# Optimization experiments

Measured on AMD Instinct MI355X. Metric: run time of the kernel, lower is better.

The kernel has to match this reference:

```python
import jax, jax.numpy as jnp
import numpy as np

VOCAB, EMB, HID = 32000, 1024, 1024
T, B = 256, 16
SIGMA = 0.01


def setup_inputs() -> dict:
    key = jax.random.key(0)
    ks = jax.random.split(key, 5)
    X = jax.random.randint(ks[0], (T, B), 0, VOCAB)
    W_e = jax.random.normal(ks[1], (VOCAB, EMB), dtype=jnp.float32) * SIGMA
    W_xh = jax.random.normal(ks[2], (EMB, HID), dtype=jnp.float32) * SIGMA
    W_hh = jax.random.normal(ks[3], (HID, HID), dtype=jnp.float32) * SIGMA
    b_h = jnp.zeros((HID,), dtype=jnp.float32)
    W_hq = jax.random.normal(ks[4], (HID, VOCAB), dtype=jnp.float32) * SIGMA
    b_q = jnp.zeros((VOCAB,), dtype=jnp.float32)
    return {"X": X, "W_e": W_e, "W_xh": W_xh, "W_hh": W_hh, "b_h": b_h,
            "W_hq": W_hq, "b_q": b_q}


def reference(X, W_e, W_xh, W_hh, b_h, W_hq, b_q):
    # one_hot(X) @ W_e is mathematically a row gather
    emb = W_e[X]  # [T, B, E]
    h0 = jnp.zeros((X.shape[1], W_hh.shape[0]), dtype=W_e.dtype)

    def step(h, x_t):
        h = jnp.tanh(x_t @ W_xh + h @ W_hh + b_h)
        return h, h

    _, hidden_states = jax.lax.scan(step, h0, emb)  # [T, B, H]
    logits = jnp.einsum('tbh,hv->tbv', hidden_states, W_hq) + b_q  # [T, B, V]
    return logits
```

## Files before the change

kernel.cpp:

```cpp
#include <hip/hip_runtime.h>
#include <hip/hip_bf16.h>
#include <stdint.h>

#define T_STEPS 256
#define BATCH   16
#define HIDDIM  1024
#define VOCAB   32000
#define TB      4096

typedef __attribute__((ext_vector_type(8))) short  short8;
typedef __attribute__((ext_vector_type(4))) float  floatx4;

__device__ inline unsigned short f2bfu(float x) {
  __hip_bfloat16 h = __float2bfloat16(x);
  unsigned short u;
  __builtin_memcpy(&u, &h, 2);
  return u;
}
__device__ inline float bfu2f(unsigned short u) {
  __hip_bfloat16 h;
  __builtin_memcpy(&h, &u, 2);
  return __bfloat162float(h);
}

__global__ __launch_bounds__(256) void transpose_cvt(
    const float* __restrict__ src, unsigned short* __restrict__ dst,
    unsigned short* __restrict__ dst_lo, int K, int N) {
  __shared__ float tile[64][65];
  int n0 = blockIdx.x * 64, k0 = blockIdx.y * 64;
  int tid = threadIdx.x;
#pragma unroll
  for (int j = 0; j < 16; ++j) {
    int idx = j * 256 + tid;
    int kl = idx >> 6, nl = idx & 63;
    tile[kl][nl] = src[(size_t)(k0 + kl) * N + n0 + nl];
  }
  __syncthreads();
#pragma unroll
  for (int j = 0; j < 16; ++j) {
    int idx = j * 256 + tid;
    int nl = idx >> 6, kl = idx & 63;
    float v = tile[kl][nl];
    unsigned short hi = f2bfu(v);
    dst[(size_t)(n0 + nl) * K + k0 + kl] = hi;
    if (dst_lo) dst_lo[(size_t)(n0 + nl) * K + k0 + kl] = f2bfu(v - bfu2f(hi));
  }
}

__global__ __launch_bounds__(256) void gather_cvt(
    const int* __restrict__ X, const float* __restrict__ We,
    unsigned short* __restrict__ emb) {
  int r = blockIdx.x;
  int row = X[r];
  int c = threadIdx.x * 4;
  float4 v = *(const float4*)(We + (size_t)row * HIDDIM + c);
  ushort4 o;
  o.x = f2bfu(v.x); o.y = f2bfu(v.y); o.z = f2bfu(v.z); o.w = f2bfu(v.w);
  *(ushort4*)(emb + (size_t)r * HIDDIM + c) = o;
}

#define BM 128
#define BN 128
#define BK 64

__device__ inline void glds16(const unsigned short* gp, unsigned short* lp) {
  __builtin_amdgcn_global_load_lds(
      (__attribute__((address_space(1))) unsigned int*)(uintptr_t)gp,
      (__attribute__((address_space(3))) unsigned int*)(unsigned int)(uintptr_t)lp,
      16, 0, 0);
}

__global__ __launch_bounds__(256) void gemm_bf16(
    const unsigned short* __restrict__ A,
    const unsigned short* __restrict__ BT,
    const float* __restrict__ bias,
    float* __restrict__ C,
    int N, int K) {
  __shared__ unsigned short As[BM * BK];
  __shared__ unsigned short Bs[BN * BK];
  int tid = threadIdx.x;
  int wave = tid >> 6, lane = tid & 63;
  int l15 = lane & 15, quad = lane >> 4;
  int m0 = blockIdx.y * BM, n0 = blockIdx.x * BN;
  int wm = (wave >> 1) * 64, wn = (wave & 1) * 64;
  int lrow = lane >> 3, lk = (lane & 7) * 8;
  floatx4 acc[4][4] = {};
  for (int kt = 0; kt < K; kt += BK) {
    __syncthreads();
#pragma unroll
    for (int i = 0; i < 4; ++i) {
      int rb = wave * 32 + i * 8;
      glds16(A  + (size_t)(m0 + rb + lrow) * K + kt + lk, As + rb * BK);
      glds16(BT + (size_t)(n0 + rb + lrow) * K + kt + lk, Bs + rb * BK);
    }
    __syncthreads();
#pragma unroll
    for (int ks = 0; ks < 2; ++ks) {
      short8 af[4], bv[4];
#pragma unroll
      for (int i = 0; i < 4; ++i)
        af[i] = *(const short8*)(As + (wm + i * 16 + l15) * BK + ks * 32 + quad * 8);
#pragma unroll
      for (int i = 0; i < 4; ++i)
        bv[i] = *(const short8*)(Bs + (wn + i * 16 + l15) * BK + ks * 32 + quad * 8);
#pragma unroll
      for (int mt = 0; mt < 4; ++mt)
#pragma unroll
        for (int nt = 0; nt < 4; ++nt)
          acc[mt][nt] = __builtin_amdgcn_mfma_f32_16x16x32_bf16(af[mt], bv[nt], acc[mt][nt], 0, 0, 0);
    }
  }
#pragma unroll
  for (int nt = 0; nt < 4; ++nt) {
    int gn = n0 + wn + nt * 16 + l15;
    float bvv = bias ? bias[gn] : 0.0f;
#pragma unroll
    for (int mt = 0; mt < 4; ++mt) {
      int gm = m0 + wm + mt * 16 + quad * 4;
#pragma unroll
      for (int r = 0; r < 4; ++r)
        C[(size_t)(gm + r) * N + gn] = acc[mt][nt][r] + bvv;
    }
  }
}

#define SCAN_WGS 64

__device__ inline short8 ld_h16_agent(const unsigned long long* p) {
  unsigned long long a = __hip_atomic_load(p,     __ATOMIC_RELAXED, __HIP_MEMORY_SCOPE_AGENT);
  unsigned long long b = __hip_atomic_load(p + 1, __ATOMIC_RELAXED, __HIP_MEMORY_SCOPE_AGENT);
  union { unsigned long long u[2]; short8 s; } c;
  c.u[0] = a; c.u[1] = b;
  return c.s;
}

__global__ __launch_bounds__(64) void scan_kernel(
    const float* __restrict__ pre,
    const unsigned short* __restrict__ WThi,
    const unsigned short* __restrict__ WTlo,
    unsigned short* __restrict__ h_hi,
    unsigned short* __restrict__ h_lo,
    unsigned int* __restrict__ flags) {
  int lane = threadIdx.x;
  int l15 = lane & 15, quad = lane >> 4;
  int wg = blockIdx.x;
  int mslice = wg * 16;
  short8 Ahi[32], Alo[32];
  {
    const unsigned short* wh = WThi + (size_t)(mslice + l15) * HIDDIM + quad * 8;
    const unsigned short* wl = WTlo + (size_t)(mslice + l15) * HIDDIM + quad * 8;
#pragma unroll
    for (int kt = 0; kt < 32; ++kt) {
      Ahi[kt] = *(const short8*)(wh + kt * 32);
      Alo[kt] = *(const short8*)(wl + kt * 32);
    }
  }
  for (int t = 0; t < T_STEPS; ++t) {
    size_t orow = ((size_t)t * BATCH + l15) * HIDDIM + mslice + quad * 4;
    float4 p = *(const float4*)(pre + orow);
    floatx4 acc = {0.f, 0.f, 0.f, 0.f};
    if (t > 0) {
      const unsigned int* fl = flags + (size_t)(t - 1) * SCAN_WGS + lane;
      int guard = 0;
      while (true) {
        unsigned int v = __hip_atomic_load(fl, __ATOMIC_RELAXED, __HIP_MEMORY_SCOPE_AGENT);
        if (__all(v != 0)) break;
        __builtin_amdgcn_s_sleep(1);
        if (++guard > (1 << 22)) break;
      }
      const unsigned long long* bh =
          (const unsigned long long*)(h_hi + ((size_t)(t - 1) * BATCH + l15) * HIDDIM + quad * 8);
      const unsigned long long* bl =
          (const unsigned long long*)(h_lo + ((size_t)(t - 1) * BATCH + l15) * HIDDIM + quad * 8);
#pragma unroll
      for (int kt = 0; kt < 32; ++kt) {
        short8 Bh = ld_h16_agent(bh + kt * 8);
        short8 Bl = ld_h16_agent(bl + kt * 8);
        acc = __builtin_amdgcn_mfma_f32_16x16x32_bf16(Ahi[kt], Bh, acc, 0, 0, 0);
        acc = __builtin_amdgcn_mfma_f32_16x16x32_bf16(Alo[kt], Bh, acc, 0, 0, 0);
        acc = __builtin_amdgcn_mfma_f32_16x16x32_bf16(Ahi[kt], Bl, acc, 0, 0, 0);
      }
    }
    ushort4 sh, sl;
    {
      float z, th; unsigned short hb;
      z = acc[0] + p.x; th = tanhf(z); hb = f2bfu(th); sh.x = hb; sl.x = f2bfu(th - bfu2f(hb));
      z = acc[1] + p.y; th = tanhf(z); hb = f2bfu(th); sh.y = hb; sl.y = f2bfu(th - bfu2f(hb));
      z = acc[2] + p.z; th = tanhf(z); hb = f2bfu(th); sh.z = hb; sl.z = f2bfu(th - bfu2f(hb));
      z = acc[3] + p.w; th = tanhf(z); hb = f2bfu(th); sh.w = hb; sl.w = f2bfu(th - bfu2f(hb));
    }
    union { ushort4 v; unsigned long long u; } ch, cl;
    ch.v = sh; cl.v = sl;
    __hip_atomic_store((unsigned long long*)(h_hi + orow), ch.u,
                       __ATOMIC_RELAXED, __HIP_MEMORY_SCOPE_AGENT);
    __hip_atomic_store((unsigned long long*)(h_lo + orow), cl.u,
                       __ATOMIC_RELAXED, __HIP_MEMORY_SCOPE_AGENT);
    __builtin_amdgcn_s_waitcnt(0);
    if (lane == 0)
      __hip_atomic_store(flags + (size_t)t * SCAN_WGS + wg, 1u,
                         __ATOMIC_RELEASE, __HIP_MEMORY_SCOPE_AGENT);
  }
}

extern "C" void kernel_launch(void* const* d_in, const int* in_sizes, int n_in,
                              void* d_out, int out_size, void* d_ws, size_t ws_size,
                              hipStream_t stream) {
  const int*   X    = (const int*)d_in[0];
  const float* W_e  = (const float*)d_in[1];
  const float* W_xh = (const float*)d_in[2];
  const float* W_hh = (const float*)d_in[3];
  const float* b_h  = (const float*)d_in[4];
  const float* W_hq = (const float*)d_in[5];
  const float* b_q  = (const float*)d_in[6];
  float* out = (float*)d_out;

  char* w = (char*)d_ws;
  unsigned short* WhqT   = (unsigned short*)(w + 0);
  unsigned short* WxhT   = (unsigned short*)(w + 65536000);
  unsigned short* WhhThi = (unsigned short*)(w + 67633152);
  unsigned short* WhhTlo = (unsigned short*)(w + 69730304);
  unsigned short* emb    = (unsigned short*)(w + 71827456);
  float*          pre    = (float*)        (w + 80216064);
  unsigned short* h_hi   = (unsigned short*)(w + 96993280);
  unsigned short* h_lo   = (unsigned short*)(w + 105381888);
  unsigned int*   flags  = (unsigned int*) (w + 113770496);

  hipMemsetAsync(flags, 0, T_STEPS * SCAN_WGS * sizeof(unsigned int), stream);
  transpose_cvt<<<dim3(VOCAB / 64, HIDDIM / 64), 256, 0, stream>>>(W_hq, WhqT, nullptr, HIDDIM, VOCAB);
  transpose_cvt<<<dim3(HIDDIM / 64, HIDDIM / 64), 256, 0, stream>>>(W_xh, WxhT, nullptr, HIDDIM, HIDDIM);
  transpose_cvt<<<dim3(HIDDIM / 64, HIDDIM / 64), 256, 0, stream>>>(W_hh, WhhThi, WhhTlo, HIDDIM, HIDDIM);
  gather_cvt<<<TB, 256, 0, stream>>>(X, W_e, emb);
  gemm_bf16<<<dim3(HIDDIM / BN, TB / BM), 256, 0, stream>>>(emb, WxhT, b_h, pre, HIDDIM, HIDDIM);
  scan_kernel<<<SCAN_WGS, 64, 0, stream>>>(pre, WhhThi, WhhTlo, h_hi, h_lo, flags);
  gemm_bf16<<<dim3(VOCAB / BN, TB / BM), 256, 0, stream>>>(h_hi, WhqT, b_q, out, VOCAB, HIDDIM);
}
```

Before: 3.993 ms.

## Replace flag sync with canary-polled fp32 hidden state and split-K waves in scan

The recurrent scan stops using per-step flags. It now writes fp32 hidden states into a buffer pre-filled with 0xFF and has consumers poll the data itself until no canary value remains. This removes the separate flag round-trip and the release/waitcnt on every step. Each workgroup now uses 4 waves that split the K dimension and reduce their partials through LDS before the tanh, which shortens the serial MFMA chain per step. The costs are a large memset, a per-load canary check, extra hi/lo conversion work on the consumer side, and reliance on tanh never producing the all-ones pattern.

```diff
diff --git a/kernel.cpp b/kernel.cpp
--- a/kernel.cpp
+++ b/kernel.cpp
@@ -125,80 +125,104 @@
 }
 
 #define SCAN_WGS 64
-
-__device__ inline short8 ld_h16_agent(const unsigned long long* p) {
-  unsigned long long a = __hip_atomic_load(p,     __ATOMIC_RELAXED, __HIP_MEMORY_SCOPE_AGENT);
-  unsigned long long b = __hip_atomic_load(p + 1, __ATOMIC_RELAXED, __HIP_MEMORY_SCOPE_AGENT);
-  union { unsigned long long u[2]; short8 s; } c;
-  c.u[0] = a; c.u[1] = b;
-  return c.s;
-}
-
-__global__ __launch_bounds__(64) void scan_kernel(
+#define CANARY64 0xFFFFFFFFFFFFFFFFull
+
+__global__ __launch_bounds__(256) void scan_kernel(
     const float* __restrict__ pre,
     const unsigned short* __restrict__ WThi,
     const unsigned short* __restrict__ WTlo,
-    unsigned short* __restrict__ h_hi,
-    unsigned short* __restrict__ h_lo,
-    unsigned int* __restrict__ flags) {
-  int lane = threadIdx.x;
+    float* __restrict__ hf,
+    unsigned short* __restrict__ h_hi) {
+  int tid = threadIdx.x;
+  int wave = tid >> 6, lane = tid & 63;
   int l15 = lane & 15, quad = lane >> 4;
   int wg = blockIdx.x;
   int mslice = wg * 16;
-  short8 Ahi[32], Alo[32];
+  int kbase = wave * 256;
+
+  short8 Ahi[8], Alo[8];
   {
-    const unsigned short* wh = WThi + (size_t)(mslice + l15) * HIDDIM + quad * 8;
-    const unsigned short* wl = WTlo + (size_t)(mslice + l15) * HIDDIM + quad * 8;
-#pragma unroll
-    for (int kt = 0; kt < 32; ++kt) {
+    const unsigned short* wh = WThi + (size_t)(mslice + l15) * HIDDIM + kbase + quad * 8;
+    const unsigned short* wl = WTlo + (size_t)(mslice + l15) * HIDDIM + kbase + quad * 8;
+#pragma unroll
+    for (int kt = 0; kt < 8; ++kt) {
       Ahi[kt] = *(const short8*)(wh + kt * 32);
       Alo[kt] = *(const short8*)(wl + kt * 32);
     }
   }
+
+  __shared__ float red[2][3][16][20];
+
   for (int t = 0; t < T_STEPS; ++t) {
-    size_t orow = ((size_t)t * BATCH + l15) * HIDDIM + mslice + quad * 4;
-    float4 p = *(const float4*)(pre + orow);
-    floatx4 acc = {0.f, 0.f, 0.f, 0.f};
+    floatx4 p;
+    size_t orow = 0;
+    if (wave == 0) {
+      orow = ((size_t)t * BATCH + l15) * HIDDIM + mslice + quad * 4;
+      p = *(const floatx4*)(pre + orow);
+    }
+    floatx4 acc0 = {0.f, 0.f, 0.f, 0.f}, acc1 = {0.f, 0.f, 0.f, 0.f};
     if (t > 0) {
-      const unsigned int* fl = flags + (size_t)(t - 1) * SCAN_WGS + lane;
+      const unsigned long long* bp = (const unsigned long long*)
+          (hf + ((size_t)(t - 1) * BATCH + l15) * HIDDIM + kbase + quad * 8);
+      unsigned long long Bw[32];
       int guard = 0;
-      while (true) {
-        unsigned int v = __hip_atomic_load(fl, __ATOMIC_RELAXED, __HIP_MEMORY_SCOPE_AGENT);
-        if (__all(v != 0)) break;
-        __builtin_amdgcn_s_sleep(1);
-        if (++guard > (1 << 22)) break;
+      bool ok;
+      do {
+        ok = true;
+#pragma unroll
+        for (int kt = 0; kt < 8; ++kt)
+#pragma unroll
+          for (int j = 0; j < 4; ++j) {
+            unsigned long long w = __hip_atomic_load(bp + (size_t)kt * 16 + j,
+                __ATOMIC_RELAXED, __HIP_MEMORY_SCOPE_AGENT);
+            Bw[kt * 4 + j] = w;
+            ok &= (w != CANARY64);
+          }
+        if (__all(ok)) break;
+        ++guard;
+        if (guard > 4) __builtin_amdgcn_s_sleep(1);
+      } while (guard <= 8192);
+#pragma unroll
+      for (int kt = 0; kt < 8; ++kt) {
+        short8 bh, bl;
+#pragma unroll
+        for (int j = 0; j < 4; ++j) {
+          unsigned long long w = Bw[kt * 4 + j];
+          unsigned int u0 = (unsigned int)w, u1 = (unsigned int)(w >> 32);
+          float f0 = __uint_as_float(u0), f1 = __uint_as_float(u1);
+          unsigned short h0 = f2bfu(f0), h1 = f2bfu(f1);
+          bh[2 * j]     = (short)h0;
+          bh[2 * j + 1] = (short)h1;
+          bl[2 * j]     = (short)f2bfu(f0 - bfu2f(h0));
+          bl[2 * j + 1] = (short)f2bfu(f1 - bfu2f(h1));
+        }
+        acc0 = __builtin_amdgcn_mfma_f32_16x16x32_bf16(Ahi[kt], bh, acc0, 0, 0, 0);
+        acc1 = __builtin_amdgcn_mfma_f32_16x16x32_bf16(Alo[kt], bh, acc1, 0, 0, 0);
+        acc0 = __builtin_amdgcn_mfma_f32_16x16x32_bf16(Ahi[kt], bl, acc0, 0, 0, 0);
       }
-      const unsigned long long* bh =
-          (const unsigned long long*)(h_hi + ((size_t)(t - 1) * BATCH + l15) * HIDDIM + quad * 8);
-      const unsigned long long* bl =
-          (const unsigned long long*)(h_lo + ((size_t)(t - 1) * BATCH + l15) * HIDDIM + quad * 8);
-#pragma unroll
-      for (int kt = 0; kt < 32; ++kt) {
-        short8 Bh = ld_h16_agent(bh + kt * 8);
-        short8 Bl = ld_h16_agent(bl + kt * 8);
-        acc = __builtin_amdgcn_mfma_f32_16x16x32_bf16(Ahi[kt], Bh, acc, 0, 0, 0);
-        acc = __builtin_amdgcn_mfma_f32_16x16x32_bf16(Alo[kt], Bh, acc, 0, 0, 0);
-        acc = __builtin_amdgcn_mfma_f32_16x16x32_bf16(Ahi[kt], Bl, acc, 0, 0, 0);
-      }
-    }
-    ushort4 sh, sl;
-    {
-      float z, th; unsigned short hb;
-      z = acc[0] + p.x; th = tanhf(z); hb = f2bfu(th); sh.x = hb; sl.x = f2bfu(th - bfu2f(hb));
-      z = acc[1] + p.y; th = tanhf(z); hb = f2bfu(th); sh.y = hb; sl.y = f2bfu(th - bfu2f(hb));
-      z = acc[2] + p.z; th = tanhf(z); hb = f2bfu(th); sh.z = hb; sl.z = f2bfu(th - bfu2f(hb));
-      z = acc[3] + p.w; th = tanhf(z); hb = f2bfu(th); sh.w = hb; sl.w = f2bfu(th - bfu2f(hb));
-    }
-    union { ushort4 v; unsigned long long u; } ch, cl;
-    ch.v = sh; cl.v = sl;
-    __hip_atomic_store((unsigned long long*)(h_hi + orow), ch.u,
-                       __ATOMIC_RELAXED, __HIP_MEMORY_SCOPE_AGENT);
-    __hip_atomic_store((unsigned long long*)(h_lo + orow), cl.u,
-                       __ATOMIC_RELAXED, __HIP_MEMORY_SCOPE_AGENT);
-    __builtin_amdgcn_s_waitcnt(0);
-    if (lane == 0)
-      __hip_atomic_store(flags + (size_t)t * SCAN_WGS + wg, 1u,
-                         __ATOMIC_RELEASE, __HIP_MEMORY_SCOPE_AGENT);
+    }
+    if (wave > 0) {
+      floatx4 s = acc0 + acc1;
+      *(floatx4*)&red[t & 1][wave - 1][l15][quad * 4] = s;
+    }
+    __syncthreads();
+    if (wave == 0) {
+      floatx4 r0 = *(const floatx4*)&red[t & 1][0][l15][quad * 4];
+      floatx4 r1 = *(const floatx4*)&red[t & 1][1][l15][quad * 4];
+      floatx4 r2 = *(const floatx4*)&red[t & 1][2][l15][quad * 4];
+      float th0 = tanhf(acc0[0] + acc1[0] + r0[0] + r1[0] + r2[0] + p[0]);
+      float th1 = tanhf(acc0[1] + acc1[1] + r0[1] + r1[1] + r2[1] + p[1]);
+      float th2 = tanhf(acc0[2] + acc1[2] + r0[2] + r1[2] + r2[2] + p[2]);
+      float th3 = tanhf(acc0[3] + acc1[3] + r0[3] + r1[3] + r2[3] + p[3]);
+      union { float f[2]; unsigned long long u; } a, b;
+      a.f[0] = th0; a.f[1] = th1; b.f[0] = th2; b.f[1] = th3;
+      unsigned long long* hp = (unsigned long long*)(hf + orow);
+      __hip_atomic_store(hp,     a.u, __ATOMIC_RELAXED, __HIP_MEMORY_SCOPE_AGENT);
+      __hip_atomic_store(hp + 1, b.u, __ATOMIC_RELAXED, __HIP_MEMORY_SCOPE_AGENT);
+      ushort4 sh;
+      sh.x = f2bfu(th0); sh.y = f2bfu(th1); sh.z = f2bfu(th2); sh.w = f2bfu(th3);
+      *(ushort4*)(h_hi + orow) = sh;
+    }
   }
 }
 
@@ -221,16 +245,15 @@
   unsigned short* WhhTlo = (unsigned short*)(w + 69730304);
   unsigned short* emb    = (unsigned short*)(w + 71827456);
   float*          pre    = (float*)        (w + 80216064);
-  unsigned short* h_hi   = (unsigned short*)(w + 96993280);
-  unsigned short* h_lo   = (unsigned short*)(w + 105381888);
-  unsigned int*   flags  = (unsigned int*) (w + 113770496);
-
-  hipMemsetAsync(flags, 0, T_STEPS * SCAN_WGS * sizeof(unsigned int), stream);
+  float*          hf     = (float*)        (w + 96993280);
+  unsigned short* h_hi   = emb;
+
+  hipMemsetAsync(hf, 0xFF, (size_t)TB * HIDDIM * sizeof(float), stream);
   transpose_cvt<<<dim3(VOCAB / 64, HIDDIM / 64), 256, 0, stream>>>(W_hq, WhqT, nullptr, HIDDIM, VOCAB);
   transpose_cvt<<<dim3(HIDDIM / 64, HIDDIM / 64), 256, 0, stream>>>(W_xh, WxhT, nullptr, HIDDIM, HIDDIM);
   transpose_cvt<<<dim3(HIDDIM / 64, HIDDIM / 64), 256, 0, stream>>>(W_hh, WhhThi, WhhTlo, HIDDIM, HIDDIM);
   gather_cvt<<<TB, 256, 0, stream>>>(X, W_e, emb);
   gemm_bf16<<<dim3(HIDDIM / BN, TB / BM), 256, 0, stream>>>(emb, WxhT, b_h, pre, HIDDIM, HIDDIM);
-  scan_kernel<<<SCAN_WGS, 64, 0, stream>>>(pre, WhhThi, WhhTlo, h_hi, h_lo, flags);
+  scan_kernel<<<SCAN_WGS, 256, 0, stream>>>(pre, WhhThi, WhhTlo, hf, h_hi);
   gemm_bf16<<<dim3(VOCAB / BN, TB / BM), 256, 0, stream>>>(h_hi, WhqT, b_q, out, VOCAB, HIDDIM);
 }
```

Measured after the change: 3.221 ms. 19.3% less time.
